# Kernel tuning notes

Hardware: AMD Instinct MI355X
Metric: run time of the kernel (lower is better)

The kernel has to match this reference:

```python
import jax, jax.numpy as jnp
import numpy as np

B, T, N, D = 2, 4, 4096, 64
DEG = 16
G = B * T                 # number of periodic structures
NNODE = G * N             # total atoms
E = NNODE * DEG           # total edges
EPS_LEN = 1e-12


def setup_inputs() -> dict:
    key = jax.random.key(0)
    ks = jax.random.split(key, 16)
    x = jax.random.normal(ks[0], (B, T, N, 3), jnp.float32) * 3.0
    x1 = jax.random.normal(ks[1], (B, T, N, 3), jnp.float32) * 3.0
    t = jax.random.uniform(ks[2], (B,), jnp.float32)
    # near-orthorhombic lattices, box size ~20 A
    cell = jnp.eye(3, dtype=jnp.float32)[None, None] * 20.0 \
        + 0.1 * jax.random.normal(ks[3], (B, T, 3, 3), jnp.float32)
    v_mask = (jax.random.uniform(ks[4], (B, T, N, 1)) > 0.1).astype(jnp.float32)
    # edges: both endpoints within the same structure's node block
    eps = E // G  # edges per structure
    local = jax.random.randint(ks[5], (2, E), 0, N, jnp.int32)
    offs = (jnp.repeat(jnp.arange(G, dtype=jnp.int32), eps) * N)[None, :]
    edge_index = local + offs
    to_jimages = jax.random.randint(ks[6], (E, 3), 0, 3, jnp.int32) - 1  # {-1,0,1}
    s = 1.0 / np.sqrt(D)
    return {
        "x": x, "t": t, "cell": cell, "x1": x1, "v_mask": v_mask,
        "W_species": jax.random.normal(ks[7], (5, D), jnp.float32) * s,
        "W_t": jax.random.normal(ks[8], (1, D), jnp.float32) * s,
        "W_edge": jax.random.normal(ks[9], (4, D), jnp.float32) * s,
        "W_msg": jax.random.normal(ks[10], (3 * D, D), jnp.float32) * s,
        "W_upd": jax.random.normal(ks[11], (D, D), jnp.float32) * s,
        "w_dec": jax.random.normal(ks[12], (D,), jnp.float32) * s,
        "edge_index": edge_index,
        "to_jimages": to_jimages,
    }


def reference(x, t, cell, x1, v_mask, W_species, W_t, W_edge, W_msg, W_upd,
              w_dec, edge_index, to_jimages):
    b, tt, n_at, _ = x.shape
    n = b * tt * n_at
    # forward(): x = x * v_mask + x1 * (1 - v_mask)  (potential_model=False)
    pos = (x * v_mask + x1 * (1.0 - v_mask)).reshape(n, 3)
    cells = cell.reshape(-1, 3, 3)                       # [G,3,3]
    src, dst = edge_index[0], edge_index[1]
    edge_graph = src // n_at                              # structure id per edge
    # get_pbc_distances: offsets = to_jimages @ cell  (per-edge gather)
    offsets = jnp.einsum('ek,ekl->el', to_jimages.astype(pos.dtype),
                         cells[edge_graph])               # [E,3]
    edge_vec = pos[dst] - pos[src] + offsets              # [E,3]
    edge_len = jnp.sqrt(jnp.sum(edge_vec * edge_vec, -1, keepdims=True) + EPS_LEN)
    edge_attr = jnp.concatenate([edge_vec, edge_len], -1)  # hstack -> [E,4]
    # per-node time feature [n,1]
    t_node = jnp.broadcast_to(t[:, None, None, None], (b, tt, n_at, 1)).reshape(n, 1)
    # species = one_hot(zeros, 5) -> [n,5]
    species = jnp.zeros((n, 5), x.dtype).at[:, 0].set(1.0)
    # encoder: scalar embedding from species + time; edge embedding; v starts at 0
    h = species @ W_species + t_node @ W_t                # [n,D]
    ea = jax.nn.silu(edge_attr @ W_edge)                  # [E,D]
    # processor: one equivariant message-passing step
    msg = jax.nn.silu(jnp.concatenate([h[src], h[dst], ea], -1) @ W_msg)  # [E,D]
    agg = jax.ops.segment_sum(msg, dst, num_segments=n)   # [n,D]
    h = h + jax.nn.silu(agg @ W_upd)
    mv = edge_vec[:, :, None] * msg[:, None, :]           # [E,3,D] vector messages
    v = jax.ops.segment_sum(mv.reshape(-1, 3 * mv.shape[-1]), dst,
                            num_segments=n).reshape(n, 3, -1)  # [n,3,D]
    # decoder: gated equivariant readout -> per-atom 3-vector
    vec_out = jnp.einsum('ncd,d->nc', v * jax.nn.silu(h)[:, None, :], w_dec)
    out = vec_out.reshape(b, tt, n_at, 3) * v_mask
    return out
```

## Files before the change

kernel.cpp:

```cpp
#include <hip/hip_runtime.h>
#include <math.h>

#define NNODE 32768
#define NEDGE 524288
#define DD 64
#define E4CAP 622592
#define SSTRIDE 77824
#define RP4S 4100

typedef float  f32x4 __attribute__((ext_vector_type(4)));
typedef short  s16x8 __attribute__((ext_vector_type(8)));
typedef short  s16x4 __attribute__((ext_vector_type(4)));

__device__ __forceinline__ float silu_f(float x) {
    return x * __builtin_amdgcn_rcpf(1.0f + __expf(-x));
}
__device__ __forceinline__ unsigned cvt_pk_bf16(float a, float b) {
    unsigned r;
    asm("v_cvt_pk_bf16_f32 %0, %1, %2" : "=v"(r) : "v"(a), "v"(b));
    return r;
}
__device__ __forceinline__ unsigned short bf16r(float f) {
    unsigned u = __float_as_uint(f);
    unsigned r = (u + 0x7FFFu + ((u >> 16) & 1u)) >> 16;
    return (unsigned short)r;
}
__device__ __forceinline__ float bf16f(unsigned short u) {
    return __uint_as_float(((unsigned)u) << 16);
}
__device__ __forceinline__ void wsync() {
    asm volatile("s_waitcnt lgkmcnt(0)" ::: "memory");
    __builtin_amdgcn_sched_barrier(0);
}

#if defined(__has_builtin) && __has_builtin(__builtin_amdgcn_mfma_f32_16x16x16bf16_1k)
#define MFMA16(a,b,c) __builtin_amdgcn_mfma_f32_16x16x16bf16_1k((a),(b),(c),0,0,0)
#else
__device__ __forceinline__ f32x4 mfma16_asm(s16x4 a, s16x4 b, f32x4 c) {
    asm("v_mfma_f32_16x16x16_bf16 %0, %1, %2, %0" : "+v"(c) : "v"(a), "v"(b));
    return c;
}
#define MFMA16(a,b,c) mfma16_asm((a),(b),(c))
#endif

__global__ __launch_bounds__(256) void k_prep_hist_base(
    const float* __restrict__ x, const float* __restrict__ x1,
    const float* __restrict__ vm, float* __restrict__ pos,
    const int* __restrict__ ei, int* __restrict__ cnt, int* __restrict__ rank,
    const float* __restrict__ Wsp, const float* __restrict__ Wt,
    const float* __restrict__ Wm, const float* __restrict__ Wu,
    const float* __restrict__ We, const float* __restrict__ tarr,
    float* __restrict__ base_ws, unsigned short* __restrict__ wfrag)
{
    int tid = threadIdx.x, b = blockIdx.x;
    if (b >= 2048) {
        if (b < 2056) {
            #pragma unroll
            for (int j = 0; j < 5; ++j) {
                int idx = (b - 2048) * 1280 + j * 256 + tid;
                unsigned short v;
                if (idx < 8192) {
                    int sel = idx >> 12, id2 = idx & 4095;
                    int jj = id2 & 7;
                    int ln = (id2 >> 3) & 63;
                    int ts = id2 >> 9;
                    int t2 = ts >> 1, s = ts & 1;
                    int k   = s*32 + (ln >> 4)*8 + jj;
                    int col = t2*16 + (ln & 15);
                    v = bf16r(sel ? Wu[k*DD + col] : Wm[(128 + k)*DD + col]);
                } else {
                    int id3 = idx - 8192;
                    int jj = id3 & 7, ln = (id3 >> 3) & 63, t2 = id3 >> 9;
                    v = (ln < 16 && jj < 4) ? bf16r(We[jj*DD + t2*16 + (ln & 15)])
                                            : (unsigned short)0;
                }
                wfrag[idx] = v;
            }
        } else if (tid < 64) {
            float t0 = tarr[0], t1 = tarr[1];
            float aA = 0.0f, aB = 0.0f;
            #pragma unroll 8
            for (int k = 0; k < DD; ++k) {
                float w = Wm[k*DD + tid] + Wm[(DD+k)*DD + tid];
                aA = fmaf(Wsp[k] + t0*Wt[k], w, aA);
                aB = fmaf(Wsp[k] + t1*Wt[k], w, aB);
            }
            base_ws[tid]      = aA;
            base_ws[DD + tid] = aB;
        }
        return;
    }
    if (b < 128) {
        int i = b*256 + tid;
        float m = vm[i];
        #pragma unroll
        for (int c = 0; c < 3; ++c)
            pos[i*3+c] = x[i*3+c]*m + x1[i*3+c]*(1.0f-m);
    }
    int e = (b & 7) * 65536 + (b >> 3) * 256 + tid;
    rank[e] = atomicAdd(&cnt[ei[NEDGE + e]], 1);
}

__global__ __launch_bounds__(1024) void k_scan(
    const int* __restrict__ cnt, int* __restrict__ rowptr, int* __restrict__ rowptr4)
{
    __shared__ int buf[2][1024];
    const int g = blockIdx.x;
    const int tid = threadIdx.x;
    int4 L = ((const int4*)cnt)[g*1024 + tid];
    int s = L.x + L.y + L.z + L.w;
    buf[0][tid] = s;
    __syncthreads();
    int pp = 0;
    for (int off = 1; off < 1024; off <<= 1) {
        int v = buf[pp][tid];
        if (tid >= off) v += buf[pp][tid - off];
        buf[pp^1][tid] = v;
        __syncthreads();
        pp ^= 1;
    }
    int ex = (tid ? buf[pp][tid-1] : 0) + g*65536;
    int4 o;
    o.x = ex; ex += L.x;
    o.y = ex; ex += L.y;
    o.z = ex; ex += L.z;
    o.w = ex; ex += L.w;
    ((int4*)rowptr)[g*1024 + tid] = o;
    if (g == 7 && tid == 1023) rowptr[32768] = NEDGE;
    __syncthreads();
    int4 P = { (L.x+3)&~3, (L.y+3)&~3, (L.z+3)&~3, (L.w+3)&~3 };
    int s4 = P.x + P.y + P.z + P.w;
    buf[0][tid] = s4;
    __syncthreads();
    pp = 0;
    for (int off = 1; off < 1024; off <<= 1) {
        int v = buf[pp][tid];
        if (tid >= off) v += buf[pp][tid - off];
        buf[pp^1][tid] = v;
        __syncthreads();
        pp ^= 1;
    }
    int ex4 = (tid ? buf[pp][tid-1] : 0) + g*SSTRIDE;
    int4 o4;
    o4.x = ex4; ex4 += P.x;
    o4.y = ex4; ex4 += P.y;
    o4.z = ex4; ex4 += P.z;
    o4.w = ex4; ex4 += P.w;
    *(int4*)(rowptr4 + g*RP4S + tid*4) = o4;
    if (tid == 1023) rowptr4[g*RP4S + 4096] = ex4;
}

__global__ __launch_bounds__(256) void k_sortgeo(
    const int* __restrict__ ei, const int* __restrict__ tj,
    const float* __restrict__ pos, const float* __restrict__ cell,
    const int* __restrict__ rowptr4, const int* __restrict__ rank,
    float4* __restrict__ srec4)
{
    int b = blockIdx.x;
    int e = (b & 7) * 65536 + (b >> 3) * 256 + threadIdx.x;
    int g = b & 7;
    int src = ei[e];
    int dst = ei[NEDGE + e];
    const float* cl = cell + g*9;
    float c00=cl[0],c01=cl[1],c02=cl[2],c10=cl[3],c11=cl[4],c12=cl[5],c20=cl[6],c21=cl[7],c22=cl[8];
    float tj0 = (float)tj[e*3+0], tj1 = (float)tj[e*3+1], tj2 = (float)tj[e*3+2];
    float ev0 = pos[dst*3+0] - pos[src*3+0] + tj0*c00 + tj1*c10 + tj2*c20;
    float ev1 = pos[dst*3+1] - pos[src*3+1] + tj0*c01 + tj1*c11 + tj2*c21;
    float ev2 = pos[dst*3+2] - pos[src*3+2] + tj0*c02 + tj1*c12 + tj2*c22;
    float len = sqrtf(ev0*ev0 + ev1*ev1 + ev2*ev2 + 1e-12f);
    int slot = rowptr4[g*RP4S + (dst & 4095)] + rank[e];
    srec4[slot] = (float4){ev0, ev1, ev2, len};
}

__global__ __launch_bounds__(64, 3) void k_edge_all(
    const float4* __restrict__ srec4,
    const int* __restrict__ rowptr, const int* __restrict__ rowptr4,
    const unsigned short* __restrict__ wfrag,
    const float* __restrict__ base_ws,
    const float* __restrict__ Wsp, const float* __restrict__ Wt,
    const float* __restrict__ wdec, const float* __restrict__ tarr,
    const float* __restrict__ vm, float* __restrict__ out)
{
    const int lane = threadIdx.x;
    const int lo16 = lane & 15;
    const int hi   = lane >> 4;
    const int grp  = (blockIdx.x & 7) * 1024 + (blockIdx.x >> 3);
    const int n0   = grp * 4;

    __shared__ __align__(16) char my[6272];
    float4*         edge4 = (float4*)my;
    unsigned short* evT   = (unsigned short*)(my + 1024);
    unsigned short* ealds = (unsigned short*)(my + 1600);
    unsigned short* agg_l = (unsigned short*)(my + 3904);
    unsigned short* v_l   = (unsigned short*)(my + 4480);

    evT[3*72 + lane] = 0x3F80;

    f32x4 accv[4][4] = {};

    s16x8 bfr[4][2], wfe[4];
    #pragma unroll
    for (int t2 = 0; t2 < 4; ++t2) {
        #pragma unroll
        for (int s = 0; s < 2; ++s)
            bfr[t2][s] = *(const s16x8*)(wfrag + ((t2*2+s)*64 + lane)*8);
        wfe[t2] = *(const s16x8*)(wfrag + 8192 + (t2*64 + lane)*8);
    }
    const bool  sb  = (n0 >> 14) != 0;
    float bv4[4];
    #pragma unroll
    for (int t2 = 0; t2 < 4; ++t2)
        bv4[t2] = base_ws[(sb ? DD : 0) + t2*16 + lo16];

    const int gS = n0 >> 12;
    const int li = gS*RP4S + (n0 & 4095);
    int rp4a[5], npad[4];
    #pragma unroll
    for (int k = 0; k <= 4; ++k)
        rp4a[k] = __builtin_amdgcn_readfirstlane(rowptr4[li + k]);
    #pragma unroll
    for (int k = 0; k < 4; ++k) {
        int r0 = __builtin_amdgcn_readfirstlane(rowptr[n0 + k]);
        int r1 = __builtin_amdgcn_readfirstlane(rowptr[n0 + k + 1]);
        npad[k] = (rp4a[k+1] - rp4a[k]) - (r1 - r0);
    }

    const int estart = rp4a[0];
    const int eend   = rp4a[4];

    int ebase = estart;
    int cnt64 = eend - ebase; if (cnt64 > 64) cnt64 = 64;
    float4 r_rec = {0.f,0.f,0.f,0.f};
    if (ebase < eend) {
        int ii = ebase + (lane < cnt64 ? lane : cnt64 - 1);
        r_rec = srec4[ii];
    }

    while (ebase < eend) {
        edge4[lane] = r_rec;
        evT[0*72 + lane] = (unsigned short)cvt_pk_bf16(r_rec.x, 0.f);
        evT[1*72 + lane] = (unsigned short)cvt_pk_bf16(r_rec.y, 0.f);
        evT[2*72 + lane] = (unsigned short)cvt_pk_bf16(r_rec.z, 0.f);

        int nb = ebase + 64;
        if (nb < eend) {
            int c2 = eend - nb; if (c2 > 64) c2 = 64;
            int jj = nb + (lane < c2 ? lane : c2 - 1);
            r_rec = srec4[jj];
        }

        int nsub = (cnt64 + 15) >> 4;
        for (int i = 0; i < nsub; ++i) {
            const int s0 = ebase + i*16;

            float4 q = edge4[i*16 + lo16];
            unsigned pa0 = cvt_pk_bf16(q.x, q.y);
            unsigned pa1 = cvt_pk_bf16(q.z, q.w);
            uint4 av = (hi == 0) ? (uint4){pa0, pa1, 0u, 0u}
                                 : (uint4){0u, 0u, 0u, 0u};
            s16x8 aea = *reinterpret_cast<s16x8*>(&av);
            #pragma unroll
            for (int t2 = 0; t2 < 4; ++t2) {
                f32x4 pre = {0.f, 0.f, 0.f, 0.f};
                pre = __builtin_amdgcn_mfma_f32_16x16x32_bf16(aea, wfe[t2], pre, 0, 0, 0);
                #pragma unroll
                for (int r = 0; r < 4; ++r)
                    ealds[(hi*4+r)*72 + t2*16 + lo16] =
                        (unsigned short)cvt_pk_bf16(silu_f(pre[r]), 0.f);
            }
            const unsigned short* arow = ealds + lo16*72 + hi*8;
            s16x8 a0 = *(const s16x8*)(arow);
            s16x8 a1 = *(const s16x8*)(arow + 32);

            s16x4 Bf[4];
            #pragma unroll
            for (int t2 = 0; t2 < 4; ++t2) {
                const float bvt = bv4[t2];
                f32x4 acc = {bvt, bvt, bvt, bvt};
                acc = __builtin_amdgcn_mfma_f32_16x16x32_bf16(a0, bfr[t2][0], acc, 0, 0, 0);
                acc = __builtin_amdgcn_mfma_f32_16x16x32_bf16(a1, bfr[t2][1], acc, 0, 0, 0);
                unsigned u0 = cvt_pk_bf16(silu_f(acc[0]), silu_f(acc[1]));
                unsigned u1 = cvt_pk_bf16(silu_f(acc[2]), silu_f(acc[3]));
                union { uint2 u2; s16x4 s4; } cv;
                cv.u2 = (uint2){u0, u1};
                Bf[t2] = cv.s4;
            }

            s16x4 a_ev = *(const s16x4*)(evT + lo16*72 + i*16 + hi*4);
            const int sc = s0 + hi*4;
            int nlv = (sc >= rp4a[1]) + (sc >= rp4a[2]) + (sc >= rp4a[3]) + (sc >= rp4a[4]);
            int nf  = (s0 >= rp4a[1]) + (s0 >= rp4a[2]) + (s0 >= rp4a[3]);
            int s3  = s0 + 12;
            int nl_ = (s3 >= rp4a[1]) + (s3 >= rp4a[2]) + (s3 >= rp4a[3]);
            s16x4 zz = {0,0,0,0};
            #pragma unroll
            for (int n = 0; n < 4; ++n) {
                if (n >= nf && n <= nl_) {
                    bool msk = (nlv == n);
                    s16x4 Am = msk ? a_ev : zz;
                    accv[n][0] = MFMA16(Am, Bf[0], accv[n][0]);
                    accv[n][1] = MFMA16(Am, Bf[1], accv[n][1]);
                    accv[n][2] = MFMA16(Am, Bf[2], accv[n][2]);
                    accv[n][3] = MFMA16(Am, Bf[3], accv[n][3]);
                }
            }
        }
        ebase = nb;
        cnt64 = eend - ebase; if (cnt64 > 64) cnt64 = 64;
    }

    float sb4[4];
    #pragma unroll
    for (int t2 = 0; t2 < 4; ++t2)
        sb4[t2] = bf16f(bf16r(silu_f(bv4[t2])));
    if (hi == 0) {
        #pragma unroll
        for (int n = 0; n < 4; ++n) {
            #pragma unroll
            for (int t2 = 0; t2 < 4; ++t2) {
                float ag = accv[n][t2][3] - (float)npad[n] * sb4[t2];
                agg_l[n*72 + t2*16 + lo16]       = (unsigned short)cvt_pk_bf16(ag, ag);
                v_l[(n*3+0)*64 + t2*16 + lo16]   = (unsigned short)cvt_pk_bf16(accv[n][t2][0], 0.f);
                v_l[(n*3+1)*64 + t2*16 + lo16]   = (unsigned short)cvt_pk_bf16(accv[n][t2][1], 0.f);
                v_l[(n*3+2)*64 + t2*16 + lo16]   = (unsigned short)cvt_pk_bf16(accv[n][t2][2], 0.f);
            }
        }
    }
    wsync();

    s16x8 wub[4][2];
    #pragma unroll
    for (int t2 = 0; t2 < 4; ++t2)
        #pragma unroll
        for (int s = 0; s < 2; ++s)
            wub[t2][s] = *(const s16x8*)(wfrag + 4096 + ((t2*2+s)*64 + lane)*8);
    const float tb = sb ? tarr[1] : tarr[0];
    float hb4[4], wd4[4];
    #pragma unroll
    for (int t2 = 0; t2 < 4; ++t2) {
        hb4[t2] = Wsp[t2*16+lo16] + tb * Wt[t2*16+lo16];
        wd4[t2] = wdec[t2*16+lo16];
    }
    s16x8 ga0 = *(const s16x8*)(agg_l + lo16*72 + hi*8);
    s16x8 ga1 = *(const s16x8*)(agg_l + lo16*72 + hi*8 + 32);
    float p[4][3] = {{0.f,0.f,0.f},{0.f,0.f,0.f},{0.f,0.f,0.f},{0.f,0.f,0.f}};
    #pragma unroll
    for (int t2 = 0; t2 < 4; ++t2) {
        f32x4 accg = {0.f, 0.f, 0.f, 0.f};
        accg = __builtin_amdgcn_mfma_f32_16x16x32_bf16(ga0, wub[t2][0], accg, 0, 0, 0);
        accg = __builtin_amdgcn_mfma_f32_16x16x32_bf16(ga1, wub[t2][1], accg, 0, 0, 0);
        #pragma unroll
        for (int r = 0; r < 4; ++r) {
            int node = hi*4 + r;
            float hn   = hb4[t2] + silu_f(accg[r]);
            float gate = silu_f(hn) * wd4[t2];
            if (node < 4) {
                #pragma unroll
                for (int c = 0; c < 3; ++c) {
                    float vv = bf16f(v_l[(node*3+c)*64 + t2*16 + lo16]);
                    p[r][c] = fmaf(gate, vv, p[r][c]);
                }
            }
        }
    }
    #pragma unroll
    for (int st = 1; st < 16; st <<= 1)
        #pragma unroll
        for (int r = 0; r < 4; ++r)
            #pragma unroll
            for (int c = 0; c < 3; ++c)
                p[r][c] += __shfl_xor(p[r][c], st, 64);

    if (lo16 < 12 && hi == 0) {
        int rr = lo16 / 3, c = lo16 - rr*3;
        float val = rr==0 ? (c==0 ? p[0][0] : c==1 ? p[0][1] : p[0][2])
                  : rr==1 ? (c==0 ? p[1][0] : c==1 ? p[1][1] : p[1][2])
                  : rr==2 ? (c==0 ? p[2][0] : c==1 ? p[2][1] : p[2][2])
                  :         (c==0 ? p[3][0] : c==1 ? p[3][1] : p[3][2]);
        out[(n0 + rr)*3 + c] = val * vm[n0 + rr];
    }
}

extern "C" void kernel_launch(void* const* d_in, const int* in_sizes, int n_in,
                              void* d_out, int out_size, void* d_ws, size_t ws_size,
                              hipStream_t stream) {
    const float* x    = (const float*)d_in[0];
    const float* t    = (const float*)d_in[1];
    const float* cell = (const float*)d_in[2];
    const float* x1   = (const float*)d_in[3];
    const float* vm   = (const float*)d_in[4];
    const float* Wsp  = (const float*)d_in[5];
    const float* Wt   = (const float*)d_in[6];
    const float* We   = (const float*)d_in[7];
    const float* Wm   = (const float*)d_in[8];
    const float* Wu   = (const float*)d_in[9];
    const float* wdec = (const float*)d_in[10];
    const int*   ei   = (const int*)d_in[11];
    const int*   tj   = (const int*)d_in[12];
    float* out = (float*)d_out;

    float*  ws      = (float*)d_ws;
    float4* srec4   = (float4*)ws;
    float*  pos     = ws + 2490368;
    int*    rank    = (int*)(pos + 98304);
    int*    rowptr  = rank + 524288;
    int*    rowptr4 = rowptr + 32772;
    int*    cnt     = rowptr4 + 32800;
    float*  base_ws = (float*)(cnt + 32768);
    unsigned short* wfrag = (unsigned short*)(base_ws + 128);

    hipMemsetAsync(cnt, 0, 32768*sizeof(int), stream);
    hipMemsetAsync(srec4, 0, (size_t)E4CAP*16, stream);
    k_prep_hist_base<<<2057, 256, 0, stream>>>(x, x1, vm, pos, ei, cnt, rank,
                                               Wsp, Wt, Wm, Wu, We, t, base_ws, wfrag);
    k_scan<<<8, 1024, 0, stream>>>(cnt, rowptr, rowptr4);
    k_sortgeo<<<2048, 256, 0, stream>>>(ei, tj, pos, cell, rowptr4, rank, srec4);
    k_edge_all<<<8192, 64, 0, stream>>>(srec4, rowptr, rowptr4, wfrag, base_ws,
                                        Wsp, Wt, wdec, t, vm, out);
}
```

Baseline: 93.25 us.

## Scatter edge vectors into per-node A rows, drop memset of padded edge records

The full memset of the padded edge-record buffer is removed. Extra blocks in the sort/geometry kernel now zero only the padding slots of each node. In the edge kernel, each edge's vector components and a constant-one column are written into the LDS A-matrix row of its destination node. This lets a single set of four MFMAs per 16-edge chunk accumulate all four nodes at once, instead of masked per-node MFMA loops, cutting MFMA count and accumulator registers. The cost is a larger LDS footprint, extra LDS zeroing each 64-edge batch, and a relaxed occupancy hint in launch bounds.

```diff
diff --git a/kernel.cpp b/kernel.cpp
--- a/kernel.cpp
+++ b/kernel.cpp
@@ -4,7 +4,6 @@
 #define NNODE 32768
 #define NEDGE 524288
 #define DD 64
-#define E4CAP 622592
 #define SSTRIDE 77824
 #define RP4S 4100
 
@@ -153,10 +152,21 @@
 __global__ __launch_bounds__(256) void k_sortgeo(
     const int* __restrict__ ei, const int* __restrict__ tj,
     const float* __restrict__ pos, const float* __restrict__ cell,
-    const int* __restrict__ rowptr4, const int* __restrict__ rank,
-    float4* __restrict__ srec4)
+    const int* __restrict__ rowptr, const int* __restrict__ rowptr4,
+    const int* __restrict__ rank, float4* __restrict__ srec4)
 {
     int b = blockIdx.x;
+    if (b >= 2048) {
+        int n  = (b - 2048) * 256 + threadIdx.x;
+        int g  = n >> 12;
+        int li = g*RP4S + (n & 4095);
+        int s0 = rowptr4[li];
+        int s1 = rowptr4[li + 1];
+        int deg = rowptr[n + 1] - rowptr[n];
+        for (int s = s0 + deg; s < s1; ++s)
+            srec4[s] = (float4){0.f, 0.f, 0.f, 0.f};
+        return;
+    }
     int e = (b & 7) * 65536 + (b >> 3) * 256 + threadIdx.x;
     int g = b & 7;
     int src = ei[e];
@@ -172,7 +182,7 @@
     srec4[slot] = (float4){ev0, ev1, ev2, len};
 }
 
-__global__ __launch_bounds__(64, 3) void k_edge_all(
+__global__ __launch_bounds__(64) void k_edge_all(
     const float4* __restrict__ srec4,
     const int* __restrict__ rowptr, const int* __restrict__ rowptr4,
     const unsigned short* __restrict__ wfrag,
@@ -187,16 +197,14 @@
     const int grp  = (blockIdx.x & 7) * 1024 + (blockIdx.x >> 3);
     const int n0   = grp * 4;
 
-    __shared__ __align__(16) char my[6272];
+    __shared__ __align__(16) char my[7936];
     float4*         edge4 = (float4*)my;
     unsigned short* evT   = (unsigned short*)(my + 1024);
-    unsigned short* ealds = (unsigned short*)(my + 1600);
-    unsigned short* agg_l = (unsigned short*)(my + 3904);
-    unsigned short* v_l   = (unsigned short*)(my + 4480);
-
-    evT[3*72 + lane] = 0x3F80;
-
-    f32x4 accv[4][4] = {};
+    unsigned short* ealds = (unsigned short*)(my + 3328);
+    unsigned short* agg_l = (unsigned short*)(my + 5632);
+    unsigned short* v_l   = (unsigned short*)(my + 6208);
+
+    f32x4 acc[4] = {};
 
     s16x8 bfr[4][2], wfe[4];
     #pragma unroll
@@ -237,10 +245,21 @@
     }
 
     while (ebase < eend) {
-        edge4[lane] = r_rec;
-        evT[0*72 + lane] = (unsigned short)cvt_pk_bf16(r_rec.x, 0.f);
-        evT[1*72 + lane] = (unsigned short)cvt_pk_bf16(r_rec.y, 0.f);
-        evT[2*72 + lane] = (unsigned short)cvt_pk_bf16(r_rec.z, 0.f);
+        float4 cur = r_rec;
+        edge4[lane] = cur;
+        {
+            int* ez = (int*)evT;
+            #pragma unroll
+            for (int j = 0; j < 9; ++j) ez[j*64 + lane] = 0;
+        }
+        if (lane < cnt64) {
+            int slot = ebase + lane;
+            int nd = (slot >= rp4a[1]) + (slot >= rp4a[2]) + (slot >= rp4a[3]);
+            evT[(nd*4+0)*72 + lane] = (unsigned short)cvt_pk_bf16(cur.x, 0.f);
+            evT[(nd*4+1)*72 + lane] = (unsigned short)cvt_pk_bf16(cur.y, 0.f);
+            evT[(nd*4+2)*72 + lane] = (unsigned short)cvt_pk_bf16(cur.z, 0.f);
+            evT[(nd*4+3)*72 + lane] = 0x3F80;
+        }
 
         int nb = ebase + 64;
         if (nb < eend) {
@@ -251,8 +270,6 @@
 
         int nsub = (cnt64 + 15) >> 4;
         for (int i = 0; i < nsub; ++i) {
-            const int s0 = ebase + i*16;
-
             float4 q = edge4[i*16 + lo16];
             unsigned pa0 = cvt_pk_bf16(q.x, q.y);
             unsigned pa1 = cvt_pk_bf16(q.z, q.w);
@@ -276,55 +293,36 @@
             #pragma unroll
             for (int t2 = 0; t2 < 4; ++t2) {
                 const float bvt = bv4[t2];
-                f32x4 acc = {bvt, bvt, bvt, bvt};
-                acc = __builtin_amdgcn_mfma_f32_16x16x32_bf16(a0, bfr[t2][0], acc, 0, 0, 0);
-                acc = __builtin_amdgcn_mfma_f32_16x16x32_bf16(a1, bfr[t2][1], acc, 0, 0, 0);
-                unsigned u0 = cvt_pk_bf16(silu_f(acc[0]), silu_f(acc[1]));
-                unsigned u1 = cvt_pk_bf16(silu_f(acc[2]), silu_f(acc[3]));
+                f32x4 am = {bvt, bvt, bvt, bvt};
+                am = __builtin_amdgcn_mfma_f32_16x16x32_bf16(a0, bfr[t2][0], am, 0, 0, 0);
+                am = __builtin_amdgcn_mfma_f32_16x16x32_bf16(a1, bfr[t2][1], am, 0, 0, 0);
+                unsigned u0 = cvt_pk_bf16(silu_f(am[0]), silu_f(am[1]));
+                unsigned u1 = cvt_pk_bf16(silu_f(am[2]), silu_f(am[3]));
                 union { uint2 u2; s16x4 s4; } cv;
                 cv.u2 = (uint2){u0, u1};
                 Bf[t2] = cv.s4;
             }
 
             s16x4 a_ev = *(const s16x4*)(evT + lo16*72 + i*16 + hi*4);
-            const int sc = s0 + hi*4;
-            int nlv = (sc >= rp4a[1]) + (sc >= rp4a[2]) + (sc >= rp4a[3]) + (sc >= rp4a[4]);
-            int nf  = (s0 >= rp4a[1]) + (s0 >= rp4a[2]) + (s0 >= rp4a[3]);
-            int s3  = s0 + 12;
-            int nl_ = (s3 >= rp4a[1]) + (s3 >= rp4a[2]) + (s3 >= rp4a[3]);
-            s16x4 zz = {0,0,0,0};
-            #pragma unroll
-            for (int n = 0; n < 4; ++n) {
-                if (n >= nf && n <= nl_) {
-                    bool msk = (nlv == n);
-                    s16x4 Am = msk ? a_ev : zz;
-                    accv[n][0] = MFMA16(Am, Bf[0], accv[n][0]);
-                    accv[n][1] = MFMA16(Am, Bf[1], accv[n][1]);
-                    accv[n][2] = MFMA16(Am, Bf[2], accv[n][2]);
-                    accv[n][3] = MFMA16(Am, Bf[3], accv[n][3]);
-                }
-            }
+            acc[0] = MFMA16(a_ev, Bf[0], acc[0]);
+            acc[1] = MFMA16(a_ev, Bf[1], acc[1]);
+            acc[2] = MFMA16(a_ev, Bf[2], acc[2]);
+            acc[3] = MFMA16(a_ev, Bf[3], acc[3]);
         }
         ebase = nb;
         cnt64 = eend - ebase; if (cnt64 > 64) cnt64 = 64;
     }
 
-    float sb4[4];
-    #pragma unroll
-    for (int t2 = 0; t2 < 4; ++t2)
-        sb4[t2] = bf16f(bf16r(silu_f(bv4[t2])));
-    if (hi == 0) {
-        #pragma unroll
-        for (int n = 0; n < 4; ++n) {
-            #pragma unroll
-            for (int t2 = 0; t2 < 4; ++t2) {
-                float ag = accv[n][t2][3] - (float)npad[n] * sb4[t2];
-                agg_l[n*72 + t2*16 + lo16]       = (unsigned short)cvt_pk_bf16(ag, ag);
-                v_l[(n*3+0)*64 + t2*16 + lo16]   = (unsigned short)cvt_pk_bf16(accv[n][t2][0], 0.f);
-                v_l[(n*3+1)*64 + t2*16 + lo16]   = (unsigned short)cvt_pk_bf16(accv[n][t2][1], 0.f);
-                v_l[(n*3+2)*64 + t2*16 + lo16]   = (unsigned short)cvt_pk_bf16(accv[n][t2][2], 0.f);
-            }
-        }
+    float npadv = hi==0 ? (float)npad[0] : hi==1 ? (float)npad[1]
+                : hi==2 ? (float)npad[2] : (float)npad[3];
+    #pragma unroll
+    for (int t2 = 0; t2 < 4; ++t2) {
+        float sbv = bf16f((unsigned short)cvt_pk_bf16(silu_f(bv4[t2]), 0.f));
+        float ag  = acc[t2][3] - npadv * sbv;
+        agg_l[hi*72 + t2*16 + lo16]       = (unsigned short)cvt_pk_bf16(ag, ag);
+        v_l[(hi*3+0)*64 + t2*16 + lo16]   = (unsigned short)cvt_pk_bf16(acc[t2][0], 0.f);
+        v_l[(hi*3+1)*64 + t2*16 + lo16]   = (unsigned short)cvt_pk_bf16(acc[t2][1], 0.f);
+        v_l[(hi*3+2)*64 + t2*16 + lo16]   = (unsigned short)cvt_pk_bf16(acc[t2][2], 0.f);
     }
     wsync();
 
@@ -410,11 +408,10 @@
     unsigned short* wfrag = (unsigned short*)(base_ws + 128);
 
     hipMemsetAsync(cnt, 0, 32768*sizeof(int), stream);
-    hipMemsetAsync(srec4, 0, (size_t)E4CAP*16, stream);
     k_prep_hist_base<<<2057, 256, 0, stream>>>(x, x1, vm, pos, ei, cnt, rank,
                                                Wsp, Wt, Wm, Wu, We, t, base_ws, wfrag);
     k_scan<<<8, 1024, 0, stream>>>(cnt, rowptr, rowptr4);
-    k_sortgeo<<<2048, 256, 0, stream>>>(ei, tj, pos, cell, rowptr4, rank, srec4);
+    k_sortgeo<<<2176, 256, 0, stream>>>(ei, tj, pos, cell, rowptr, rowptr4, rank, srec4);
     k_edge_all<<<8192, 64, 0, stream>>>(srec4, rowptr, rowptr4, wfrag, base_ws,
                                         Wsp, Wt, wdec, t, vm, out);
 }
```

Result: faster. 81.89 us (-12.2%).
